# Optimization experiments

Measured on AMD Instinct MI355X. Metric: run time of the kernel, lower is better.

## Reference

```python
import jax, jax.numpy as jnp
import numpy as np

N_NODES = 8_000_000
N_GRAPHS = 16384
OUT_DIM = 256
LABEL_MAX = 300  # some labels >= OUT_DIM to exercise the bounds check


def setup_inputs() -> dict:
    key = jax.random.key(0)
    k1, k2 = jax.random.split(key)
    x = jax.random.randint(k1, (N_NODES,), 0, LABEL_MAX, dtype=jnp.int32)
    # ptr: sorted segment boundaries with ptr[0]=0, ptr[-1]=N_NODES
    inner = jnp.sort(jax.random.randint(k2, (N_GRAPHS - 1,), 0, N_NODES, dtype=jnp.int32))
    ptr = jnp.concatenate([jnp.zeros((1,), jnp.int32), inner,
                           jnp.full((1,), N_NODES, jnp.int32)])
    node_weights = jnp.ones((N_NODES,), jnp.float32)  # all-ones -> plain counting
    return {"x": x, "ptr": ptr, "node_weights": node_weights,
            "num_graphs": N_GRAPHS, "out_dim": OUT_DIM}


def reference(x, ptr, node_weights, num_graphs, out_dim):
    # Segmented histogram: out[g, c] = # nodes in graph g with label c (c < out_dim).
    n = x.shape[0]
    # graph id of each node from CSR ptr boundaries
    seg = jnp.searchsorted(ptr, jnp.arange(n, dtype=ptr.dtype), side="right") - 1
    valid = x < out_dim
    xc = jnp.where(valid, x, 0)                 # clamp out-of-range labels
    w = jnp.where(valid, node_weights, 0.0)     # mask them out of the count
    out = jnp.zeros((num_graphs, out_dim), jnp.float32).at[seg, xc].add(w)
    return out
```

## Files before the change

### kernel.cpp

```cpp
#include <hip/hip_runtime.h>


#define CHUNK   2048
#define BLOCK_B 256

extern "C" __global__ __launch_bounds__(64)
void setup_kernel(const int* __restrict__ ptr, int* __restrict__ gstart,
                  float* __restrict__ out, int n_nodes, int num_graphs,
                  int out_dim) {
    const int b = blockIdx.x;
    long n0 = (long)b * CHUNK;
    if (n0 > (long)n_nodes - 1) n0 = (long)n_nodes - 1;

    int lo = 0, hi = num_graphs + 1;
    while (lo < hi) {
        const int mid = (lo + hi) >> 1;
        if ((long)ptr[mid] <= n0) lo = mid + 1; else hi = mid;
    }
    const int g = lo - 1;

    if (threadIdx.x == 0) gstart[b] = g;

    float* row = out + (size_t)g * (size_t)out_dim;
    for (int c = (int)threadIdx.x; c < out_dim; c += 64) row[c] = 0.0f;
}

extern "C" __global__ __launch_bounds__(BLOCK_B)
void hist_kernel(const int* __restrict__ x, const int* __restrict__ ptr,
                 const float* __restrict__ w, const int* __restrict__ gstart,
                 float* __restrict__ out, int n_nodes, int out_dim) {
    extern __shared__ char smem[];
    int*   xbuf = (int*)smem;
    float* wbuf = (float*)(smem + CHUNK * sizeof(int));
    float* hist = (float*)(smem + CHUNK * sizeof(int) + CHUNK * sizeof(float));

    const int b   = blockIdx.x;
    const int t   = (int)threadIdx.x;
    const int n0  = b * CHUNK;
    const int n1  = min(n0 + CHUNK, n_nodes);
    const int cnt = n1 - n0;

    for (int base = 0; base < cnt; base += 4 * BLOCK_B) {
        const int idx = base + t * 4;
        if (idx + 4 <= cnt) {
            *reinterpret_cast<int4*>(&xbuf[idx])   = *reinterpret_cast<const int4*>(&x[n0 + idx]);
            *reinterpret_cast<float4*>(&wbuf[idx]) = *reinterpret_cast<const float4*>(&w[n0 + idx]);
        } else if (idx < cnt) {
            for (int k = idx; k < cnt; ++k) { xbuf[k] = x[n0 + k]; wbuf[k] = w[n0 + k]; }
        }
    }

    const int g0 = gstart[b];
    const int g1 = gstart[b + 1];
    __syncthreads();

    int pjs = ptr[g0];
    for (int j = g0; j <= g1; ++j) {
        const int pje = ptr[j + 1];
        const int s = max(pjs, n0) - n0;
        const int e = min(pje, n1) - n0;

        for (int c = t; c < out_dim; c += BLOCK_B) hist[c] = 0.0f;
        __syncthreads();

        for (int i = s + t; i < e; i += BLOCK_B) {
            const unsigned lbl = (unsigned)xbuf[i];
            if (lbl < (unsigned)out_dim) atomicAdd(&hist[lbl], wbuf[i]);
        }
        __syncthreads();

        float* row = out + (size_t)j * (size_t)out_dim;
        if (j == g0 || j == g1) {
            for (int c = t; c < out_dim; c += BLOCK_B) {
                const float v = hist[c];
                if (v != 0.0f) atomicAdd(&row[c], v);
            }
        } else {
            for (int c = t; c < out_dim; c += BLOCK_B) row[c] = hist[c];
        }
        pjs = pje;
    }
}

extern "C" __global__ __launch_bounds__(256)
void seg_hist_fallback(const int* __restrict__ x, const int* __restrict__ ptr,
                       const float* __restrict__ w, float* __restrict__ out,
                       int out_dim) {
    extern __shared__ float fhist[];
    const int g = blockIdx.x;
    const int start = ptr[g];
    const int end = ptr[g + 1];
    for (int c = (int)threadIdx.x; c < out_dim; c += 256) fhist[c] = 0.0f;
    __syncthreads();
    for (int i = start + (int)threadIdx.x; i < end; i += 256) {
        const int lbl = x[i];
        if ((unsigned)lbl < (unsigned)out_dim) atomicAdd(&fhist[lbl], w[i]);
    }
    __syncthreads();
    float* o = out + (size_t)g * (size_t)out_dim;
    for (int c = (int)threadIdx.x; c < out_dim; c += 256) o[c] = fhist[c];
}

extern "C" void kernel_launch(void* const* d_in, const int* in_sizes, int n_in,
                              void* d_out, int out_size, void* d_ws, size_t ws_size,
                              hipStream_t stream) {
    const int* x   = (const int*)d_in[0];
    const int* ptr = (const int*)d_in[1];
    const float* w = (const float*)d_in[2];
    float* out     = (float*)d_out;

    const int n_nodes    = in_sizes[0];
    const int num_graphs = in_sizes[1] - 1;
    const int out_dim    = out_size / num_graphs;
    const int n_chunks   = (n_nodes + CHUNK - 1) / CHUNK;

    if (ws_size < (size_t)(n_chunks + 1) * sizeof(int)) {
        seg_hist_fallback<<<num_graphs, 256, (size_t)out_dim * sizeof(float), stream>>>(
            x, ptr, w, out, out_dim);
        return;
    }

    int* gstart = (int*)d_ws;

    setup_kernel<<<n_chunks + 1, 64, 0, stream>>>(ptr, gstart, out,
                                                  n_nodes, num_graphs, out_dim);

    const size_t lds = (size_t)CHUNK * 8 + (size_t)out_dim * sizeof(float);
    hist_kernel<<<n_chunks, BLOCK_B, lds, stream>>>(x, ptr, w, gstart, out,
                                                    n_nodes, out_dim);
}
```

Measured before the change: 57.45 us.

## Keep node chunk in registers instead of LDS staging, specialize out_dim

Each thread now loads its 8 consecutive labels and weights straight into registers with vector loads, rather than staging the whole 2048-node chunk in shared memory. Only the 256-float histogram stays in LDS. The histogram is sized at compile time for out_dim 256, and each graph's reset is folded into its write-out step. Waves whose slice does not overlap a graph's range skip the atomic step. This removes 16KB of LDS per block, which should raise occupancy (launch bounds now request 6 blocks) and cut the LDS copy traffic. Any out_dim other than 256 now goes to the slow fallback path.

```diff
diff --git a/kernel.cpp b/kernel.cpp
--- a/kernel.cpp
+++ b/kernel.cpp
@@ -2,7 +2,9 @@
 
 
 #define CHUNK   2048
+#define NPT     8
 #define BLOCK_B 256
+#define ODIM    256
 
 extern "C" __global__ __launch_bounds__(64)
 void setup_kernel(const int* __restrict__ ptr, int* __restrict__ gstart,
@@ -25,59 +27,78 @@
     for (int c = (int)threadIdx.x; c < out_dim; c += 64) row[c] = 0.0f;
 }
 
-extern "C" __global__ __launch_bounds__(BLOCK_B)
+extern "C" __global__ __launch_bounds__(BLOCK_B, 6)
 void hist_kernel(const int* __restrict__ x, const int* __restrict__ ptr,
                  const float* __restrict__ w, const int* __restrict__ gstart,
-                 float* __restrict__ out, int n_nodes, int out_dim) {
-    extern __shared__ char smem[];
-    int*   xbuf = (int*)smem;
-    float* wbuf = (float*)(smem + CHUNK * sizeof(int));
-    float* hist = (float*)(smem + CHUNK * sizeof(int) + CHUNK * sizeof(float));
+                 float* __restrict__ out, int n_nodes, int num_graphs) {
+    __shared__ float hist[ODIM];
 
-    const int b   = blockIdx.x;
-    const int t   = (int)threadIdx.x;
-    const int n0  = b * CHUNK;
-    const int n1  = min(n0 + CHUNK, n_nodes);
-    const int cnt = n1 - n0;
+    const int b  = blockIdx.x;
+    const int t  = (int)threadIdx.x;
+    const int n0 = b * CHUNK;
+    const int n1 = min(n0 + CHUNK, n_nodes);
 
-    for (int base = 0; base < cnt; base += 4 * BLOCK_B) {
-        const int idx = base + t * 4;
-        if (idx + 4 <= cnt) {
-            *reinterpret_cast<int4*>(&xbuf[idx])   = *reinterpret_cast<const int4*>(&x[n0 + idx]);
-            *reinterpret_cast<float4*>(&wbuf[idx]) = *reinterpret_cast<const float4*>(&w[n0 + idx]);
-        } else if (idx < cnt) {
-            for (int k = idx; k < cnt; ++k) { xbuf[k] = x[n0 + k]; wbuf[k] = w[n0 + k]; }
+    const int base = n0 + t * NPT;
+    int4 la, lb; float4 wa, wb;
+    if (base + NPT <= n1) {
+        la = *reinterpret_cast<const int4*>(x + base);
+        lb = *reinterpret_cast<const int4*>(x + base + 4);
+        wa = *reinterpret_cast<const float4*>(w + base);
+        wb = *reinterpret_cast<const float4*>(w + base + 4);
+    } else {
+        int l[NPT]; float ww[NPT];
+#pragma unroll
+        for (int k = 0; k < NPT; ++k) {
+            if (base + k < n1) { l[k] = x[base + k]; ww[k] = w[base + k]; }
+            else               { l[k] = 0x7fffffff;  ww[k] = 0.0f; }
         }
+        la = make_int4(l[0], l[1], l[2], l[3]);
+        lb = make_int4(l[4], l[5], l[6], l[7]);
+        wa = make_float4(ww[0], ww[1], ww[2], ww[3]);
+        wb = make_float4(ww[4], ww[5], ww[6], ww[7]);
     }
 
     const int g0 = gstart[b];
     const int g1 = gstart[b + 1];
+    int jbeg = g0, jend = g1;
+    if (b == 0) jbeg = 0;
+    if (b == (int)gridDim.x - 1) jend = num_graphs - 1;
+
+    hist[t] = 0.0f;
     __syncthreads();
 
-    int pjs = ptr[g0];
-    for (int j = g0; j <= g1; ++j) {
+    const int i0    = t * NPT;
+    const int wbase = (t & ~63) * NPT;
+
+    int pjs = ptr[jbeg];
+    for (int j = jbeg; j <= jend; ++j) {
         const int pje = ptr[j + 1];
         const int s = max(pjs, n0) - n0;
         const int e = min(pje, n1) - n0;
 
-        for (int c = t; c < out_dim; c += BLOCK_B) hist[c] = 0.0f;
-        __syncthreads();
-
-        for (int i = s + t; i < e; i += BLOCK_B) {
-            const unsigned lbl = (unsigned)xbuf[i];
-            if (lbl < (unsigned)out_dim) atomicAdd(&hist[lbl], wbuf[i]);
+        if (s < e && e > wbase && s < wbase + 64 * NPT) {
+#define ADDK(LBL, WV, K)                                               \
+            { const int ii = i0 + (K);                                 \
+              if (ii >= s && ii < e && (unsigned)(LBL) < (unsigned)ODIM) \
+                  atomicAdd(&hist[LBL], (WV)); }
+            ADDK(la.x, wa.x, 0) ADDK(la.y, wa.y, 1)
+            ADDK(la.z, wa.z, 2) ADDK(la.w, wa.w, 3)
+            ADDK(lb.x, wb.x, 4) ADDK(lb.y, wb.y, 5)
+            ADDK(lb.z, wb.z, 6) ADDK(lb.w, wb.w, 7)
+#undef ADDK
         }
         __syncthreads();
 
-        float* row = out + (size_t)j * (size_t)out_dim;
+        float* row = out + (size_t)j * ODIM;
+        const float v = hist[t];
         if (j == g0 || j == g1) {
-            for (int c = t; c < out_dim; c += BLOCK_B) {
-                const float v = hist[c];
-                if (v != 0.0f) atomicAdd(&row[c], v);
-            }
+            if (v != 0.0f) atomicAdd(&row[t], v);
         } else {
-            for (int c = t; c < out_dim; c += BLOCK_B) row[c] = hist[c];
+            row[t] = v;
         }
+        hist[t] = 0.0f;
+        __syncthreads();
+
         pjs = pje;
     }
 }
@@ -114,7 +135,7 @@
     const int out_dim    = out_size / num_graphs;
     const int n_chunks   = (n_nodes + CHUNK - 1) / CHUNK;
 
-    if (ws_size < (size_t)(n_chunks + 1) * sizeof(int)) {
+    if (out_dim != ODIM || ws_size < (size_t)(n_chunks + 1) * sizeof(int)) {
         seg_hist_fallback<<<num_graphs, 256, (size_t)out_dim * sizeof(float), stream>>>(
             x, ptr, w, out, out_dim);
         return;
@@ -125,7 +146,6 @@
     setup_kernel<<<n_chunks + 1, 64, 0, stream>>>(ptr, gstart, out,
                                                   n_nodes, num_graphs, out_dim);
 
-    const size_t lds = (size_t)CHUNK * 8 + (size_t)out_dim * sizeof(float);
-    hist_kernel<<<n_chunks, BLOCK_B, lds, stream>>>(x, ptr, w, gstart, out,
-                                                    n_nodes, out_dim);
+    hist_kernel<<<n_chunks, BLOCK_B, 0, stream>>>(x, ptr, w, gstart, out,
+                                                  n_nodes, num_graphs);
 }
```

After: 55.17 us. 1.04x faster.
